# Optimization experiments

Hardware: AMD Instinct MI355X
Metric: run time of the kernel (lower is better)

## Reference

```python
import jax, jax.numpy as jnp
import numpy as np

M, N, DIM = 128, 128, 2048
NITER = 1000
ALPHA = 0.3
SIGMA = max(M, N) / 2.0  # 64.0
PDIST_EPS = 1e-6         # nn.PairwiseDistance default eps (added to the difference)


def setup_inputs() -> dict:
    key = jax.random.key(0)
    k1, k2 = jax.random.split(key)
    x = jax.random.normal(k1, (DIM,), dtype=jnp.float32)
    weights = jax.random.normal(k2, (M * N, DIM), dtype=jnp.float32)
    # neuron_locations(): row-major (i, j) grid over m x n
    ii, jj = jnp.meshgrid(jnp.arange(M), jnp.arange(N), indexing="ij")
    locations = jnp.stack([ii.reshape(-1), jj.reshape(-1)], axis=1).astype(jnp.int64)  # (m*n, 2)
    it = 100
    return {"x": x, "weights": weights, "locations": locations, "it": it}


def reference(x, weights, locations, it):
    # --- BMU search: PairwiseDistance(p=2) between broadcast x and all weights ---
    diff = x[None, :] - weights + PDIST_EPS            # (m*n, dim)
    dists = jnp.sqrt(jnp.sum(diff * diff, axis=1))     # (m*n,)
    bmu_index = jnp.argmin(dists)                      # first min, like torch.min
    bmu_loc = locations[bmu_index]                     # (2,)
    # NOTE: original code uses bmu_loc[0]*m + bmu_loc[1] (m, not n) — kept faithful
    bmu_loc_1d = bmu_loc[0] * M + bmu_loc[1]

    # --- linearly decaying learning rate / sigma ---
    lr = 1.0 - it / NITER
    alpha_op = ALPHA * lr
    sigma_op = SIGMA * lr

    # --- Gaussian neighbourhood around BMU ---
    loc_diff = locations.astype(jnp.float32) - bmu_loc.astype(jnp.float32)  # (m*n, 2)
    bmu_dist_sq = jnp.sum(loc_diff * loc_diff, axis=1)                      # (m*n,)
    neighbourhood = jnp.exp(-bmu_dist_sq / (sigma_op ** 2))                 # (m*n,)
    rate = alpha_op * neighbourhood                                         # (m*n,)

    # --- weight update ---
    delta = rate[:, None] * (x[None, :] - weights)     # (m*n, dim)
    new_weights = weights + delta
    return new_weights
```

## Files before the change

### kernel.cpp

```cpp
#include <hip/hip_runtime.h>
#include <hip/hip_bf16.h>


#define ROWS 16384
#define NBLK 1024
#define NWAVES 4096
#define RPW 4
#define EPS 1e-6f

typedef float fx4 __attribute__((ext_vector_type(4)));
typedef unsigned long long u64;

__global__ __launch_bounds__(256) void som_argmin(const float* __restrict__ x,
                                                  const float* __restrict__ w,
                                                  u64* __restrict__ key) {
    const int lane = threadIdx.x & 63;
    const int wid  = threadIdx.x >> 6;
    const int gw   = blockIdx.x * 4 + wid;

    fx4 xv[8];
#pragma unroll
    for (int i = 0; i < 8; ++i) xv[i] = ((const fx4*)x)[lane + i * 64];

    fx4 wv[RPW][8];
#pragma unroll
    for (int r = 0; r < RPW; ++r) {
        const fx4* wr = (const fx4*)(w + (size_t)(gw + r * NWAVES) * 2048);
#pragma unroll
        for (int i = 0; i < 8; ++i) wv[r][i] = wr[lane + i * 64];
    }

    u64 best = ~0ULL;
#pragma unroll
    for (int r = 0; r < RPW; ++r) {
        float acc = 0.0f;
#pragma unroll
        for (int i = 0; i < 8; ++i) {
            fx4 d = xv[i] - wv[r][i] + EPS;
            acc += d.x * d.x + d.y * d.y + d.z * d.z + d.w * d.w;
        }
#pragma unroll
        for (int off = 32; off > 0; off >>= 1) acc += __shfl_xor(acc, off);
        u64 k = ((u64)__float_as_uint(acc) << 32) | (unsigned)(gw + r * NWAVES);
        best = best < k ? best : k;
    }

    __shared__ u64 sk[4];
    if (lane == 0) sk[wid] = best;
    __syncthreads();
    if (threadIdx.x == 0) {
        u64 b0 = sk[0] < sk[1] ? sk[0] : sk[1];
        u64 b1 = sk[2] < sk[3] ? sk[2] : sk[3];
        u64 b  = b0 < b1 ? b0 : b1;
        atomicMin(key, b);
    }
}

__global__ __launch_bounds__(256) void som_update(const float* __restrict__ x,
                                                  const float* __restrict__ w,
                                                  const u64* __restrict__ key,
                                                  const int* __restrict__ itp,
                                                  float* __restrict__ out) {
    const int lane = threadIdx.x & 63;
    const int wid  = threadIdx.x >> 6;
    const int gw   = blockIdx.x * 4 + wid;

    const int bmu = (int)(unsigned)(*key & 0xFFFFFFFFULL);
    const float bi = (float)(bmu >> 7);
    const float bj = (float)(bmu & 127);

    const float lr       = 1.0f - (float)(*itp) / 1000.0f;
    const float alpha_op = 0.3f * lr;
    const float sigma_op = 64.0f * lr;
    const float s2       = sigma_op * sigma_op;

    fx4 xv[8];
#pragma unroll
    for (int i = 0; i < 8; ++i) xv[i] = ((const fx4*)x)[lane + i * 64];

    float rate[RPW];
#pragma unroll
    for (int r = 0; r < RPW; ++r) {
        const int row = gw + r * NWAVES;
        const float di = (float)(row >> 7) - bi;
        const float dj = (float)(row & 127) - bj;
        const float gd2 = di * di + dj * dj;
        rate[r] = alpha_op * expf(-(gd2 / s2));
    }

    fx4 wv[RPW][8];
#pragma unroll
    for (int r = 0; r < RPW; ++r) {
        const fx4* wr = (const fx4*)(w + (size_t)(gw + r * NWAVES) * 2048);
#pragma unroll
        for (int i = 0; i < 8; ++i) wv[r][i] = wr[lane + i * 64];
    }

#pragma unroll
    for (int r = 0; r < RPW; ++r) {
        fx4* orow = (fx4*)(out + (size_t)(gw + r * NWAVES) * 2048);
#pragma unroll
        for (int i = 0; i < 8; ++i)
            orow[lane + i * 64] = wv[r][i] + rate[r] * (xv[i] - wv[r][i]);
    }
}

extern "C" void kernel_launch(void* const* d_in, const int* in_sizes, int n_in,
                              void* d_out, int out_size, void* d_ws, size_t ws_size,
                              hipStream_t stream) {
    const float* x = (const float*)d_in[0];
    const float* w = (const float*)d_in[1];
    const int* itp = (const int*)d_in[3];
    float* out = (float*)d_out;
    u64* key = (u64*)d_ws;

    hipMemsetAsync(d_ws, 0xFF, sizeof(u64), stream);

    som_argmin<<<NBLK, 256, 0, stream>>>(x, w, key);
    som_update<<<NBLK, 256, 0, stream>>>(x, w, key, itp, out);
}
```

Baseline: 262.4 us.

## Spread argmin atomics across padded slots, halve rows per wave, nontemporal output stores

The argmin kernel now writes its per-block minimum to one of 64 padded slots instead of a single global key, which cuts contention on one atomic. The update kernel reduces those slots with a wave shuffle before use. The grid doubles so each wave handles 2 rows instead of 4, giving more parallelism and lower register pressure. The update kernel also issues its weight loads before reading the key and writes output with nontemporal stores to limit cache pollution, at the cost of an extra 64-entry reduction per wave.

```diff
diff --git a/kernel.cpp b/kernel.cpp
--- a/kernel.cpp
+++ b/kernel.cpp
@@ -3,17 +3,20 @@
 
 
 #define ROWS 16384
-#define NBLK 1024
-#define NWAVES 4096
-#define RPW 4
+#define NBLK 2048
+#define NWAVES 8192
 #define EPS 1e-6f
+#define KSLOTS 64
+#define KPAD 8
 
 typedef float fx4 __attribute__((ext_vector_type(4)));
 typedef unsigned long long u64;
 
+__device__ __forceinline__ u64 u64min(u64 a, u64 b) { return a < b ? a : b; }
+
 __global__ __launch_bounds__(256) void som_argmin(const float* __restrict__ x,
                                                   const float* __restrict__ w,
-                                                  u64* __restrict__ key) {
+                                                  u64* __restrict__ keys) {
     const int lane = threadIdx.x & 63;
     const int wid  = threadIdx.x >> 6;
     const int gw   = blockIdx.x * 4 + wid;
@@ -22,50 +25,72 @@
 #pragma unroll
     for (int i = 0; i < 8; ++i) xv[i] = ((const fx4*)x)[lane + i * 64];
 
-    fx4 wv[RPW][8];
+    const fx4* r0 = (const fx4*)(w + (size_t)gw * 2048);
+    const fx4* r1 = (const fx4*)(w + (size_t)(gw + NWAVES) * 2048);
+    fx4 a[8], b[8];
 #pragma unroll
-    for (int r = 0; r < RPW; ++r) {
-        const fx4* wr = (const fx4*)(w + (size_t)(gw + r * NWAVES) * 2048);
+    for (int i = 0; i < 8; ++i) a[i] = r0[lane + i * 64];
 #pragma unroll
-        for (int i = 0; i < 8; ++i) wv[r][i] = wr[lane + i * 64];
+    for (int i = 0; i < 8; ++i) b[i] = r1[lane + i * 64];
+
+    float acc0 = 0.0f, acc1 = 0.0f;
+#pragma unroll
+    for (int i = 0; i < 8; ++i) {
+        fx4 d = xv[i] - a[i] + EPS;
+        acc0 += d.x * d.x + d.y * d.y + d.z * d.z + d.w * d.w;
+    }
+#pragma unroll
+    for (int i = 0; i < 8; ++i) {
+        fx4 d = xv[i] - b[i] + EPS;
+        acc1 += d.x * d.x + d.y * d.y + d.z * d.z + d.w * d.w;
+    }
+#pragma unroll
+    for (int off = 32; off > 0; off >>= 1) {
+        acc0 += __shfl_xor(acc0, off);
+        acc1 += __shfl_xor(acc1, off);
     }
 
-    u64 best = ~0ULL;
-#pragma unroll
-    for (int r = 0; r < RPW; ++r) {
-        float acc = 0.0f;
-#pragma unroll
-        for (int i = 0; i < 8; ++i) {
-            fx4 d = xv[i] - wv[r][i] + EPS;
-            acc += d.x * d.x + d.y * d.y + d.z * d.z + d.w * d.w;
-        }
-#pragma unroll
-        for (int off = 32; off > 0; off >>= 1) acc += __shfl_xor(acc, off);
-        u64 k = ((u64)__float_as_uint(acc) << 32) | (unsigned)(gw + r * NWAVES);
-        best = best < k ? best : k;
-    }
+    u64 k0 = ((u64)__float_as_uint(acc0) << 32) | (unsigned)gw;
+    u64 k1 = ((u64)__float_as_uint(acc1) << 32) | (unsigned)(gw + NWAVES);
+    u64 best = u64min(k0, k1);
 
     __shared__ u64 sk[4];
     if (lane == 0) sk[wid] = best;
     __syncthreads();
     if (threadIdx.x == 0) {
-        u64 b0 = sk[0] < sk[1] ? sk[0] : sk[1];
-        u64 b1 = sk[2] < sk[3] ? sk[2] : sk[3];
-        u64 b  = b0 < b1 ? b0 : b1;
-        atomicMin(key, b);
+        u64 m = u64min(u64min(sk[0], sk[1]), u64min(sk[2], sk[3]));
+        atomicMin(&keys[(blockIdx.x & (KSLOTS - 1)) * KPAD], m);
     }
 }
 
 __global__ __launch_bounds__(256) void som_update(const float* __restrict__ x,
                                                   const float* __restrict__ w,
-                                                  const u64* __restrict__ key,
+                                                  const u64* __restrict__ keys,
                                                   const int* __restrict__ itp,
                                                   float* __restrict__ out) {
     const int lane = threadIdx.x & 63;
     const int wid  = threadIdx.x >> 6;
     const int gw   = blockIdx.x * 4 + wid;
 
-    const int bmu = (int)(unsigned)(*key & 0xFFFFFFFFULL);
+    const fx4* r0 = (const fx4*)(w + (size_t)gw * 2048);
+    const fx4* r1 = (const fx4*)(w + (size_t)(gw + NWAVES) * 2048);
+    fx4 a[8], b[8];
+#pragma unroll
+    for (int i = 0; i < 8; ++i) a[i] = r0[lane + i * 64];
+#pragma unroll
+    for (int i = 0; i < 8; ++i) b[i] = r1[lane + i * 64];
+
+    fx4 xv[8];
+#pragma unroll
+    for (int i = 0; i < 8; ++i) xv[i] = ((const fx4*)x)[lane + i * 64];
+
+    u64 k = keys[lane * KPAD];
+#pragma unroll
+    for (int off = 32; off > 0; off >>= 1) {
+        u64 o = __shfl_xor(k, off);
+        k = o < k ? o : k;
+    }
+    const int bmu = (int)(unsigned)(k & 0xFFFFFFFFULL);
     const float bi = (float)(bmu >> 7);
     const float bj = (float)(bmu & 127);
 
@@ -74,34 +99,23 @@
     const float sigma_op = 64.0f * lr;
     const float s2       = sigma_op * sigma_op;
 
-    fx4 xv[8];
+    const int row0 = gw, row1 = gw + NWAVES;
+    float di0 = (float)(row0 >> 7) - bi, dj0 = (float)(row0 & 127) - bj;
+    float di1 = (float)(row1 >> 7) - bi, dj1 = (float)(row1 & 127) - bj;
+    const float rate0 = alpha_op * expf(-((di0 * di0 + dj0 * dj0) / s2));
+    const float rate1 = alpha_op * expf(-((di1 * di1 + dj1 * dj1) / s2));
+
+    fx4* o0 = (fx4*)(out + (size_t)row0 * 2048);
+    fx4* o1 = (fx4*)(out + (size_t)row1 * 2048);
 #pragma unroll
-    for (int i = 0; i < 8; ++i) xv[i] = ((const fx4*)x)[lane + i * 64];
-
-    float rate[RPW];
+    for (int i = 0; i < 8; ++i) {
+        fx4 v = a[i] + rate0 * (xv[i] - a[i]);
+        __builtin_nontemporal_store(v, &o0[lane + i * 64]);
+    }
 #pragma unroll
-    for (int r = 0; r < RPW; ++r) {
-        const int row = gw + r * NWAVES;
-        const float di = (float)(row >> 7) - bi;
-        const float dj = (float)(row & 127) - bj;
-        const float gd2 = di * di + dj * dj;
-        rate[r] = alpha_op * expf(-(gd2 / s2));
-    }
-
-    fx4 wv[RPW][8];
-#pragma unroll
-    for (int r = 0; r < RPW; ++r) {
-        const fx4* wr = (const fx4*)(w + (size_t)(gw + r * NWAVES) * 2048);
-#pragma unroll
-        for (int i = 0; i < 8; ++i) wv[r][i] = wr[lane + i * 64];
-    }
-
-#pragma unroll
-    for (int r = 0; r < RPW; ++r) {
-        fx4* orow = (fx4*)(out + (size_t)(gw + r * NWAVES) * 2048);
-#pragma unroll
-        for (int i = 0; i < 8; ++i)
-            orow[lane + i * 64] = wv[r][i] + rate[r] * (xv[i] - wv[r][i]);
+    for (int i = 0; i < 8; ++i) {
+        fx4 v = b[i] + rate1 * (xv[i] - b[i]);
+        __builtin_nontemporal_store(v, &o1[lane + i * 64]);
     }
 }
 
@@ -112,10 +126,10 @@
     const float* w = (const float*)d_in[1];
     const int* itp = (const int*)d_in[3];
     float* out = (float*)d_out;
-    u64* key = (u64*)d_ws;
+    u64* keys = (u64*)d_ws;
 
-    hipMemsetAsync(d_ws, 0xFF, sizeof(u64), stream);
+    hipMemsetAsync(d_ws, 0xFF, KSLOTS * KPAD * sizeof(u64), stream);
 
-    som_argmin<<<NBLK, 256, 0, stream>>>(x, w, key);
-    som_update<<<NBLK, 256, 0, stream>>>(x, w, key, itp, out);
+    som_argmin<<<NBLK, 256, 0, stream>>>(x, w, keys);
+    som_update<<<NBLK, 256, 0, stream>>>(x, w, keys, itp, out);
 }
```

Measured after the change: 256.9 us. -2.1%, faster.
